# Performance work log

Measured on AMD Instinct MI355X. Metric: run time of the kernel, lower is better.

The kernel has to match this reference:

```python
import jax, jax.numpy as jnp
import numpy as np

N, D, E = 32768, 768, 8
F = 4 * D  # 3072


def setup_inputs() -> dict:
    key = jax.random.key(0)
    ks = jax.random.split(key, 8)
    scale = 0.02
    hidden_states = jax.random.normal(ks[0], (N, D), dtype=jnp.float32)
    Wg = jax.random.normal(ks[1], (E, D), dtype=jnp.float32) * scale  # gate, no bias
    W1 = jax.random.normal(ks[2], (E, F, D), dtype=jnp.float32) * scale
    b1 = jnp.zeros((E, F), dtype=jnp.float32)
    W2 = jax.random.normal(ks[3], (E, D, F), dtype=jnp.float32) * scale
    b2 = jnp.zeros((E, D), dtype=jnp.float32)
    W3 = jax.random.normal(ks[4], (E, 1, D), dtype=jnp.float32) * scale
    b3 = jnp.zeros((E, 1), dtype=jnp.float32)
    return {"hidden_states": hidden_states, "Wg": Wg, "W1": W1, "b1": b1,
            "W2": W2, "b2": b2, "W3": W3, "b3": b3, "top_k": 2}


def reference(hidden_states, Wg, W1, b1, W2, b2, W3, b3, top_k):
    x = hidden_states  # [N, D]
    logits = x @ Wg.T  # [N, E]
    probs = jax.nn.softmax(logits.astype(jnp.float32), axis=-1)
    w, _sel = jax.lax.top_k(probs, top_k)  # [N, k] (descending)
    w = (w / w.sum(axis=-1, keepdims=True)).astype(x.dtype)
    # FAITHFUL TO SOURCE BUG: expert used is the position index j (experts[j]),
    # not the selected expert id. So densely run experts 0..top_k-1 on all tokens.
    W1k, b1k = W1[:top_k], b1[:top_k]
    W2k, b2k = W2[:top_k], b2[:top_k]
    W3k, b3k = W3[:top_k], b3[:top_k]
    # dropout is identity in eval mode
    h = jax.nn.relu(jnp.einsum('nd,kfd->knf', x, W1k) + b1k[:, None, :])  # [k,N,F]
    o = x[None, :, :] + jnp.einsum('knf,kdf->knd', h, W2k) + b2k[:, None, :]  # residual, [k,N,D]
    s = jnp.einsum('knd,kod->kno', o, W3k) + b3k[:, None, :]  # [k,N,1]
    out = jnp.sum(jnp.swapaxes(w, 0, 1)[:, :, None] * s, axis=0)  # [N,1]
    return out
```

## Files before the change

kernel.cpp:

```cpp
#include <hip/hip_runtime.h>
#include <hip/hip_bf16.h>
#include <stdint.h>

#define N_TOK 32768
#define DDIM  768
#define FDIM  3072
#define NCOLS (2*FDIM)
#define BK    64
#define KTILES (DDIM/BK)
#define NTILES (NCOLS/256)
#define VD_CHUNK 96

typedef __attribute__((ext_vector_type(8))) short bf16x8;
typedef __attribute__((ext_vector_type(4))) float f32x4;

__device__ __forceinline__ unsigned short f2bf(float f) {
  unsigned u = __builtin_bit_cast(unsigned, f);
  unsigned r = (u + 0x7fffu + ((u >> 16) & 1u)) >> 16;
  return (unsigned short)r;
}

__device__ __forceinline__ void gl_lds16(const void* g, void* l) {
  __builtin_amdgcn_global_load_lds(
      (const __attribute__((address_space(1))) unsigned int*)g,
      (__attribute__((address_space(3))) unsigned int*)l, 16, 0, 0);
}

__global__ __launch_bounds__(256) void cvt_kernel(const float* __restrict__ src,
                                                  unsigned short* __restrict__ dst) {
  size_t i = ((size_t)blockIdx.x * 256 + threadIdx.x) * 4;
  float4 f = *(const float4*)(src + i);
  ushort4 u;
  u.x = f2bf(f.x); u.y = f2bf(f.y); u.z = f2bf(f.z); u.w = f2bf(f.w);
  *(ushort4*)(dst + i) = u;
}

__global__ __launch_bounds__(256) void vcalc_kernel(const float* __restrict__ W2,
                                                    const float* __restrict__ W3,
                                                    float* __restrict__ vpart) {
  __shared__ float w3s[VD_CHUNK];
  int k  = blockIdx.x / 12;
  int fb = blockIdx.x % 12;
  int db = blockIdx.y;
  if (threadIdx.x < VD_CHUNK) w3s[threadIdx.x] = W3[k*DDIM + db*VD_CHUNK + threadIdx.x];
  __syncthreads();
  int f = fb*256 + threadIdx.x;
  const float* W2k = W2 + (size_t)k*DDIM*FDIM + (size_t)db*VD_CHUNK*FDIM + f;
  float s = 0.f;
  #pragma unroll 8
  for (int d = 0; d < VD_CHUNK; ++d) s += W2k[(size_t)d*FDIM] * w3s[d];
  vpart[(size_t)db*NCOLS + k*FDIM + f] = s;
}

__global__ __launch_bounds__(256) void vfinal_kernel(const float* __restrict__ vpart,
                                                     float* __restrict__ v,
                                                     const float* __restrict__ b2,
                                                     const float* __restrict__ W3,
                                                     const float* __restrict__ b3,
                                                     float* __restrict__ cbuf) {
  int f = blockIdx.x*256 + threadIdx.x;
  float s = 0.f;
  #pragma unroll
  for (int db = 0; db < 8; ++db) s += vpart[(size_t)db*NCOLS + f];
  v[f] = s;
  if (blockIdx.x == 0 && threadIdx.x < 128) {
    int k = threadIdx.x >> 6, lane = threadIdx.x & 63;
    float c = 0.f;
    #pragma unroll
    for (int it = 0; it < DDIM/64; ++it) {
      int i = it*64 + lane;
      c += b2[k*DDIM + i] * W3[k*DDIM + i];
    }
    #pragma unroll
    for (int m = 1; m < 64; m <<= 1) c += __shfl_xor(c, m, 64);
    if (lane == 0) cbuf[k] = c + b3[k];
  }
}

__global__ __launch_bounds__(256) void gate_cvt_kernel(
    const float* __restrict__ x, const float* __restrict__ Wg,
    const float* __restrict__ W3, const float* __restrict__ cbuf,
    unsigned short* __restrict__ xbf,
    float* __restrict__ wgt, float* __restrict__ base) {
  int wid  = threadIdx.x >> 6;
  int lane = threadIdx.x & 63;
  int n = blockIdx.x * 4 + wid;
  const float4* xr = (const float4*)(x + (size_t)n * DDIM);
  ushort4* xw = (ushort4*)(xbf + (size_t)n * DDIM);
  float acc[8] = {0,0,0,0,0,0,0,0};
  float d30 = 0.f, d31 = 0.f;
  #pragma unroll
  for (int it = 0; it < DDIM/256; ++it) {
    int i = it*64 + lane;
    float4 xv = xr[i];
    ushort4 u;
    u.x = f2bf(xv.x); u.y = f2bf(xv.y); u.z = f2bf(xv.z); u.w = f2bf(xv.w);
    xw[i] = u;
    #pragma unroll
    for (int e = 0; e < 8; ++e) {
      float4 w = ((const float4*)(Wg + e*DDIM))[i];
      acc[e] += xv.x*w.x + xv.y*w.y + xv.z*w.z + xv.w*w.w;
    }
    float4 wa = ((const float4*)W3)[i];
    d30 += xv.x*wa.x + xv.y*wa.y + xv.z*wa.z + xv.w*wa.w;
    float4 wb = ((const float4*)(W3 + DDIM))[i];
    d31 += xv.x*wb.x + xv.y*wb.y + xv.z*wb.z + xv.w*wb.w;
  }
  #pragma unroll
  for (int m = 1; m < 64; m <<= 1) {
    #pragma unroll
    for (int e = 0; e < 8; ++e) acc[e] += __shfl_xor(acc[e], m, 64);
    d30 += __shfl_xor(d30, m, 64);
    d31 += __shfl_xor(d31, m, 64);
  }
  if (lane == 0) {
    float l1 = acc[0]; int a1 = 0;
    #pragma unroll
    for (int e = 1; e < 8; ++e) if (acc[e] > l1) { l1 = acc[e]; a1 = e; }
    float l2 = -3.4e38f;
    #pragma unroll
    for (int e = 0; e < 8; ++e) if (e != a1 && acc[e] > l2) l2 = acc[e];
    float w0 = 1.f / (1.f + __expf(l2 - l1));
    float w1 = 1.f - w0;
    wgt[2*n]   = w0;
    wgt[2*n+1] = w1;
    base[n] = w0 * (d30 + cbuf[0]) + w1 * (d31 + cbuf[1]);
  }
}

__global__ __launch_bounds__(512, 2) void gemm_kernel(
    const unsigned short* __restrict__ A,
    const unsigned short* __restrict__ B,
    const float* __restrict__ b1,
    const float* __restrict__ v,
    float* __restrict__ part) {
  __shared__ __align__(16) char smem[131072];

  const int tid  = threadIdx.x;
  const int lane = tid & 63, wid = tid >> 6;
  const int wm = wid >> 2, wn = wid & 3;
  const int q  = lane >> 4, cl = lane & 15;

  const int b  = blockIdx.x;
  const int L  = (b & 7) * 384 + (b >> 3);
  const int bn = L % 24;
  const int bm = L / 24;

  const unsigned short* Ab = A + (size_t)bm * 256 * DDIM;
  const unsigned short* Bb = B + (size_t)bn * 256 * DDIM;

  const size_t srow = (size_t)(wid*16 + cl) * DDIM + q*8;

  const int lb = lane * 16;
  const int aBase = wm*8192 + lb;
  const int bBase = 16384 + wn*4096 + lb;

  f32x4 zero = {0.f, 0.f, 0.f, 0.f};
  f32x4 acc[8][4];
  #pragma unroll
  for (int i = 0; i < 8; ++i)
    #pragma unroll
    for (int j = 0; j < 4; ++j) acc[i][j] = zero;

  auto stageA = [&](int t, int ks) {
    char* dst = smem + (t & 1) * 65536 + ks * 32768;
    const unsigned short* s0 = Ab + srow + t*BK + ks*32;
    gl_lds16(s0,            dst + wid*1024);
    gl_lds16(s0 + 128*DDIM, dst + 8192 + wid*1024);
  };
  auto stageB = [&](int t, int ks) {
    char* dst = smem + (t & 1) * 65536 + ks * 32768 + 16384;
    const unsigned short* s0 = Bb + srow + t*BK + ks*32;
    gl_lds16(s0,            dst + wid*1024);
    gl_lds16(s0 + 128*DDIM, dst + 8192 + wid*1024);
  };

  stageA(0, 0); stageB(0, 0);
  stageA(0, 1); stageB(0, 1);
  stageA(1, 0); stageB(1, 0);
  asm volatile("s_waitcnt vmcnt(8)" ::: "memory");
  __builtin_amdgcn_s_barrier();
  __builtin_amdgcn_sched_barrier(0);

  #pragma unroll
  for (int kt = 0; kt < KTILES; ++kt) {
    const char* ct = smem + (kt & 1) * 65536;
    bf16x8 a0[4], a1[4], bf0[4];

    #pragma unroll
    for (int n = 0; n < 4; ++n) bf0[n] = *(const bf16x8*)(ct + bBase + n*1024);
    #pragma unroll
    for (int m = 0; m < 4; ++m) a0[m] = *(const bf16x8*)(ct + aBase + m*1024);
    #pragma unroll
    for (int m = 0; m < 4; ++m) a1[m] = *(const bf16x8*)(ct + aBase + 4096 + m*1024);
    if (kt <= 10) { stageA(kt + 1, 1); stageB(kt + 1, 1); }
    __builtin_amdgcn_s_setprio(1);
    #pragma unroll
    for (int m = 0; m < 4; ++m)
      #pragma unroll
      for (int n = 0; n < 4; ++n)
        acc[m][n] = __builtin_amdgcn_mfma_f32_16x16x32_bf16(a0[m], bf0[n], acc[m][n], 0, 0, 0);
    #pragma unroll
    for (int m = 0; m < 4; ++m)
      #pragma unroll
      for (int n = 0; n < 4; ++n)
        acc[4 + m][n] = __builtin_amdgcn_mfma_f32_16x16x32_bf16(a1[m], bf0[n], acc[4 + m][n], 0, 0, 0);
    __builtin_amdgcn_s_setprio(0);
    if (kt <= 10) { asm volatile("s_waitcnt vmcnt(8)" ::: "memory"); }
    else          { asm volatile("s_waitcnt vmcnt(0)" ::: "memory"); }
    __builtin_amdgcn_s_barrier();
    __builtin_amdgcn_sched_barrier(0);

    #pragma unroll
    for (int n = 0; n < 4; ++n) bf0[n] = *(const bf16x8*)(ct + 32768 + bBase + n*1024);
    #pragma unroll
    for (int m = 0; m < 4; ++m) a0[m] = *(const bf16x8*)(ct + 32768 + aBase + m*1024);
    #pragma unroll
    for (int m = 0; m < 4; ++m) a1[m] = *(const bf16x8*)(ct + 32768 + aBase + 4096 + m*1024);
    if (kt <= 9) { stageA(kt + 2, 0); stageB(kt + 2, 0); }
    __builtin_amdgcn_s_setprio(1);
    #pragma unroll
    for (int m = 0; m < 4; ++m)
      #pragma unroll
      for (int n = 0; n < 4; ++n)
        acc[m][n] = __builtin_amdgcn_mfma_f32_16x16x32_bf16(a0[m], bf0[n], acc[m][n], 0, 0, 0);
    #pragma unroll
    for (int m = 0; m < 4; ++m)
      #pragma unroll
      for (int n = 0; n < 4; ++n)
        acc[4 + m][n] = __builtin_amdgcn_mfma_f32_16x16x32_bf16(a1[m], bf0[n], acc[4 + m][n], 0, 0, 0);
    __builtin_amdgcn_s_setprio(0);
    if (kt <= 9)       { asm volatile("s_waitcnt vmcnt(8)" ::: "memory"); }
    else if (kt == 10) { asm volatile("s_waitcnt vmcnt(4)" ::: "memory"); }
    __builtin_amdgcn_s_barrier();
    __builtin_amdgcn_sched_barrier(0);
  }

  float vv[4], bb[4];
  #pragma unroll
  for (int n = 0; n < 4; ++n) {
    int cg = bn*256 + wn*64 + n*16 + cl;
    vv[n] = v[cg];
    bb[n] = b1[cg];
  }
  float* red = (float*)smem;
  #pragma unroll
  for (int mt = 0; mt < 8; ++mt) {
    #pragma unroll
    for (int rr = 0; rr < 4; ++rr) {
      float s = 0.f;
      #pragma unroll
      for (int n = 0; n < 4; ++n) {
        float val = acc[mt][n][rr] + bb[n];
        s += fmaxf(val, 0.f) * vv[n];
      }
      #pragma unroll
      for (int msk = 1; msk < 16; msk <<= 1) s += __shfl_xor(s, msk, 64);
      if (cl == 0) red[(wm*128 + mt*16 + q*4 + rr)*4 + wn] = s;
    }
  }
  __syncthreads();
  if (tid < 256) {
    float r4 = red[tid*4] + red[tid*4+1] + red[tid*4+2] + red[tid*4+3];
    part[(size_t)bn * N_TOK + (size_t)bm*256 + tid] = r4;
  }
}

__global__ __launch_bounds__(256) void final_kernel(const float* __restrict__ part,
                                                    const float* __restrict__ wgt,
                                                    const float* __restrict__ base,
                                                    float* __restrict__ out) {
  int n = blockIdx.x * 256 + threadIdx.x;
  float s0 = 0.f, s1 = 0.f;
  #pragma unroll
  for (int t = 0; t < 12; ++t) s0 += part[(size_t)t*N_TOK + n];
  #pragma unroll
  for (int t = 12; t < 24; ++t) s1 += part[(size_t)t*N_TOK + n];
  out[n] = base[n] + wgt[2*n]*s0 + wgt[2*n+1]*s1;
}

extern "C" void kernel_launch(void* const* d_in, const int* in_sizes, int n_in,
                              void* d_out, int out_size, void* d_ws, size_t ws_size,
                              hipStream_t stream) {
  const float* x  = (const float*)d_in[0];
  const float* Wg = (const float*)d_in[1];
  const float* W1 = (const float*)d_in[2];
  const float* b1 = (const float*)d_in[3];
  const float* W2 = (const float*)d_in[4];
  const float* b2 = (const float*)d_in[5];
  const float* W3 = (const float*)d_in[6];
  const float* b3 = (const float*)d_in[7];
  float* out = (float*)d_out;

  char* ws = (char*)d_ws;
  size_t off = 0;
  auto alloc = [&](size_t bytes) -> char* {
    char* p = ws + off;
    off += (bytes + 255) & ~(size_t)255;
    return p;
  };
  unsigned short* xbf  = (unsigned short*)alloc((size_t)N_TOK * DDIM * 2);
  unsigned short* w1bf = (unsigned short*)alloc((size_t)NCOLS * DDIM * 2);
  float* vpart = (float*)alloc((size_t)8 * NCOLS * 4);
  float* v     = (float*)alloc((size_t)NCOLS * 4);
  float* cbuf  = (float*)alloc(64);
  float* wgt   = (float*)alloc((size_t)N_TOK * 2 * 4);
  float* base  = (float*)alloc((size_t)N_TOK * 4);
  float* part  = (float*)alloc((size_t)NTILES * N_TOK * 4);
  if (off > ws_size) return;

  cvt_kernel<<<(NCOLS*DDIM)/1024, 256, 0, stream>>>(W1, w1bf);
  vcalc_kernel<<<dim3(24, 8), 256, 0, stream>>>(W2, W3, vpart);
  vfinal_kernel<<<NCOLS/256, 256, 0, stream>>>(vpart, v, b2, W3, b3, cbuf);
  gate_cvt_kernel<<<N_TOK/4, 256, 0, stream>>>(x, Wg, W3, cbuf, xbf, wgt, base);
  gemm_kernel<<<3072, 512, 0, stream>>>(xbf, w1bf, b1, v, part);
  final_kernel<<<N_TOK/256, 256, 0, stream>>>(part, wgt, base, out);
}
```

Before: 626.6 us.

## Fuse prep kernels into one launch, split LDS waits in GEMM, simplify grid

```diff
diff --git a/kernel.cpp b/kernel.cpp
--- a/kernel.cpp
+++ b/kernel.cpp
@@ -11,6 +11,11 @@
 #define NTILES (NCOLS/256)
 #define VD_CHUNK 96
 
+#define CVT_BLOCKS   4608
+#define VCALC_BLOCKS 192
+#define GATE_BLOCKS  8192
+#define PREP_BLOCKS  (CVT_BLOCKS + VCALC_BLOCKS + 1 + GATE_BLOCKS)
+
 typedef __attribute__((ext_vector_type(8))) short bf16x8;
 typedef __attribute__((ext_vector_type(4))) float f32x4;
 
@@ -26,65 +31,60 @@
       (__attribute__((address_space(3))) unsigned int*)l, 16, 0, 0);
 }
 
-__global__ __launch_bounds__(256) void cvt_kernel(const float* __restrict__ src,
-                                                  unsigned short* __restrict__ dst) {
-  size_t i = ((size_t)blockIdx.x * 256 + threadIdx.x) * 4;
-  float4 f = *(const float4*)(src + i);
-  ushort4 u;
-  u.x = f2bf(f.x); u.y = f2bf(f.y); u.z = f2bf(f.z); u.w = f2bf(f.w);
-  *(ushort4*)(dst + i) = u;
-}
-
-__global__ __launch_bounds__(256) void vcalc_kernel(const float* __restrict__ W2,
-                                                    const float* __restrict__ W3,
-                                                    float* __restrict__ vpart) {
-  __shared__ float w3s[VD_CHUNK];
-  int k  = blockIdx.x / 12;
-  int fb = blockIdx.x % 12;
-  int db = blockIdx.y;
-  if (threadIdx.x < VD_CHUNK) w3s[threadIdx.x] = W3[k*DDIM + db*VD_CHUNK + threadIdx.x];
-  __syncthreads();
-  int f = fb*256 + threadIdx.x;
-  const float* W2k = W2 + (size_t)k*DDIM*FDIM + (size_t)db*VD_CHUNK*FDIM + f;
-  float s = 0.f;
-  #pragma unroll 8
-  for (int d = 0; d < VD_CHUNK; ++d) s += W2k[(size_t)d*FDIM] * w3s[d];
-  vpart[(size_t)db*NCOLS + k*FDIM + f] = s;
-}
-
-__global__ __launch_bounds__(256) void vfinal_kernel(const float* __restrict__ vpart,
-                                                     float* __restrict__ v,
-                                                     const float* __restrict__ b2,
-                                                     const float* __restrict__ W3,
-                                                     const float* __restrict__ b3,
-                                                     float* __restrict__ cbuf) {
-  int f = blockIdx.x*256 + threadIdx.x;
-  float s = 0.f;
-  #pragma unroll
-  for (int db = 0; db < 8; ++db) s += vpart[(size_t)db*NCOLS + f];
-  v[f] = s;
-  if (blockIdx.x == 0 && threadIdx.x < 128) {
-    int k = threadIdx.x >> 6, lane = threadIdx.x & 63;
-    float c = 0.f;
-    #pragma unroll
-    for (int it = 0; it < DDIM/64; ++it) {
-      int i = it*64 + lane;
-      c += b2[k*DDIM + i] * W3[k*DDIM + i];
-    }
-    #pragma unroll
-    for (int m = 1; m < 64; m <<= 1) c += __shfl_xor(c, m, 64);
-    if (lane == 0) cbuf[k] = c + b3[k];
-  }
-}
-
-__global__ __launch_bounds__(256) void gate_cvt_kernel(
+__global__ __launch_bounds__(256) void prep_kernel(
+    const float* __restrict__ W1, unsigned short* __restrict__ w1bf,
+    const float* __restrict__ W2, const float* __restrict__ W3,
+    float* __restrict__ v,
+    const float* __restrict__ b2, const float* __restrict__ b3,
+    float* __restrict__ cbuf,
     const float* __restrict__ x, const float* __restrict__ Wg,
-    const float* __restrict__ W3, const float* __restrict__ cbuf,
     unsigned short* __restrict__ xbf,
     float* __restrict__ wgt, float* __restrict__ base) {
+  __shared__ float w3s[VD_CHUNK];
+  const int b = blockIdx.x;
+
+  if (b < CVT_BLOCKS) {
+    size_t i = ((size_t)b * 256 + threadIdx.x) * 4;
+    float4 f = *(const float4*)(W1 + i);
+    ushort4 u;
+    u.x = f2bf(f.x); u.y = f2bf(f.y); u.z = f2bf(f.z); u.w = f2bf(f.w);
+    *(ushort4*)(w1bf + i) = u;
+    return;
+  }
+  if (b < CVT_BLOCKS + VCALC_BLOCKS) {
+    int vb = b - CVT_BLOCKS;
+    int k  = vb / 96;
+    int fb = (vb % 96) / 8;
+    int db = vb % 8;
+    if (threadIdx.x < VD_CHUNK) w3s[threadIdx.x] = W3[k*DDIM + db*VD_CHUNK + threadIdx.x];
+    __syncthreads();
+    int f = fb*256 + threadIdx.x;
+    const float* W2k = W2 + (size_t)k*DDIM*FDIM + (size_t)db*VD_CHUNK*FDIM + f;
+    float s = 0.f;
+    #pragma unroll 8
+    for (int d = 0; d < VD_CHUNK; ++d) s += W2k[(size_t)d*FDIM] * w3s[d];
+    atomicAdd(&v[k*FDIM + f], s);
+    return;
+  }
+  if (b == CVT_BLOCKS + VCALC_BLOCKS) {
+    if (threadIdx.x < 128) {
+      int k = threadIdx.x >> 6, lane = threadIdx.x & 63;
+      float c = 0.f;
+      #pragma unroll
+      for (int it = 0; it < DDIM/64; ++it) {
+        int i = it*64 + lane;
+        c += b2[k*DDIM + i] * W3[k*DDIM + i];
+      }
+      #pragma unroll
+      for (int m = 1; m < 64; m <<= 1) c += __shfl_xor(c, m, 64);
+      if (lane == 0) cbuf[k] = c + b3[k];
+    }
+    return;
+  }
+  int gb   = b - (CVT_BLOCKS + VCALC_BLOCKS + 1);
   int wid  = threadIdx.x >> 6;
   int lane = threadIdx.x & 63;
-  int n = blockIdx.x * 4 + wid;
+  int n = gb * 4 + wid;
   const float4* xr = (const float4*)(x + (size_t)n * DDIM);
   ushort4* xw = (ushort4*)(xbf + (size_t)n * DDIM);
   float acc[8] = {0,0,0,0,0,0,0,0};
@@ -124,7 +124,7 @@
     float w1 = 1.f - w0;
     wgt[2*n]   = w0;
     wgt[2*n+1] = w1;
-    base[n] = w0 * (d30 + cbuf[0]) + w1 * (d31 + cbuf[1]);
+    base[n] = w0 * d30 + w1 * d31;
   }
 }
 
@@ -140,11 +140,8 @@
   const int lane = tid & 63, wid = tid >> 6;
   const int wm = wid >> 2, wn = wid & 3;
   const int q  = lane >> 4, cl = lane & 15;
-
-  const int b  = blockIdx.x;
-  const int L  = (b & 7) * 384 + (b >> 3);
-  const int bn = L % 24;
-  const int bm = L / 24;
+  const int bn = blockIdx.x;
+  const int bm = blockIdx.y;
 
   const unsigned short* Ab = A + (size_t)bm * 256 * DDIM;
   const unsigned short* Bb = B + (size_t)bn * 256 * DDIM;
@@ -185,26 +182,32 @@
   #pragma unroll
   for (int kt = 0; kt < KTILES; ++kt) {
     const char* ct = smem + (kt & 1) * 65536;
-    bf16x8 a0[4], a1[4], bf0[4];
-
-    #pragma unroll
-    for (int n = 0; n < 4; ++n) bf0[n] = *(const bf16x8*)(ct + bBase + n*1024);
+    bf16x8 a0[4], a1[4], bfr[4];
+
+    #pragma unroll
+    for (int n = 0; n < 4; ++n) bfr[n] = *(const bf16x8*)(ct + bBase + n*1024);
     #pragma unroll
     for (int m = 0; m < 4; ++m) a0[m] = *(const bf16x8*)(ct + aBase + m*1024);
     #pragma unroll
     for (int m = 0; m < 4; ++m) a1[m] = *(const bf16x8*)(ct + aBase + 4096 + m*1024);
     if (kt <= 10) { stageA(kt + 1, 1); stageB(kt + 1, 1); }
+    asm volatile("s_waitcnt lgkmcnt(4)" ::: "memory");
+    __builtin_amdgcn_sched_barrier(0);
     __builtin_amdgcn_s_setprio(1);
     #pragma unroll
     for (int m = 0; m < 4; ++m)
       #pragma unroll
       for (int n = 0; n < 4; ++n)
-        acc[m][n] = __builtin_amdgcn_mfma_f32_16x16x32_bf16(a0[m], bf0[n], acc[m][n], 0, 0, 0);
+        acc[m][n] = __builtin_amdgcn_mfma_f32_16x16x32_bf16(a0[m], bfr[n], acc[m][n], 0, 0, 0);
+    __builtin_amdgcn_s_setprio(0);
+    asm volatile("s_waitcnt lgkmcnt(0)" ::: "memory");
+    __builtin_amdgcn_sched_barrier(0);
+    __builtin_amdgcn_s_setprio(1);
     #pragma unroll
     for (int m = 0; m < 4; ++m)
       #pragma unroll
       for (int n = 0; n < 4; ++n)
-        acc[4 + m][n] = __builtin_amdgcn_mfma_f32_16x16x32_bf16(a1[m], bf0[n], acc[4 + m][n], 0, 0, 0);
+        acc[4 + m][n] = __builtin_amdgcn_mfma_f32_16x16x32_bf16(a1[m], bfr[n], acc[4 + m][n], 0, 0, 0);
     __builtin_amdgcn_s_setprio(0);
     if (kt <= 10) { asm volatile("s_waitcnt vmcnt(8)" ::: "memory"); }
     else          { asm volatile("s_waitcnt vmcnt(0)" ::: "memory"); }
@@ -212,23 +215,29 @@
     __builtin_amdgcn_sched_barrier(0);
 
     #pragma unroll
-    for (int n = 0; n < 4; ++n) bf0[n] = *(const bf16x8*)(ct + 32768 + bBase + n*1024);
+    for (int n = 0; n < 4; ++n) bfr[n] = *(const bf16x8*)(ct + 32768 + bBase + n*1024);
     #pragma unroll
     for (int m = 0; m < 4; ++m) a0[m] = *(const bf16x8*)(ct + 32768 + aBase + m*1024);
     #pragma unroll
     for (int m = 0; m < 4; ++m) a1[m] = *(const bf16x8*)(ct + 32768 + aBase + 4096 + m*1024);
     if (kt <= 9) { stageA(kt + 2, 0); stageB(kt + 2, 0); }
+    asm volatile("s_waitcnt lgkmcnt(4)" ::: "memory");
+    __builtin_amdgcn_sched_barrier(0);
     __builtin_amdgcn_s_setprio(1);
     #pragma unroll
     for (int m = 0; m < 4; ++m)
       #pragma unroll
       for (int n = 0; n < 4; ++n)
-        acc[m][n] = __builtin_amdgcn_mfma_f32_16x16x32_bf16(a0[m], bf0[n], acc[m][n], 0, 0, 0);
+        acc[m][n] = __builtin_amdgcn_mfma_f32_16x16x32_bf16(a0[m], bfr[n], acc[m][n], 0, 0, 0);
+    __builtin_amdgcn_s_setprio(0);
+    asm volatile("s_waitcnt lgkmcnt(0)" ::: "memory");
+    __builtin_amdgcn_sched_barrier(0);
+    __builtin_amdgcn_s_setprio(1);
     #pragma unroll
     for (int m = 0; m < 4; ++m)
       #pragma unroll
       for (int n = 0; n < 4; ++n)
-        acc[4 + m][n] = __builtin_amdgcn_mfma_f32_16x16x32_bf16(a1[m], bf0[n], acc[4 + m][n], 0, 0, 0);
+        acc[4 + m][n] = __builtin_amdgcn_mfma_f32_16x16x32_bf16(a1[m], bfr[n], acc[4 + m][n], 0, 0, 0);
     __builtin_amdgcn_s_setprio(0);
     if (kt <= 9)       { asm volatile("s_waitcnt vmcnt(8)" ::: "memory"); }
     else if (kt == 10) { asm volatile("s_waitcnt vmcnt(4)" ::: "memory"); }
@@ -269,6 +278,7 @@
 __global__ __launch_bounds__(256) void final_kernel(const float* __restrict__ part,
                                                     const float* __restrict__ wgt,
                                                     const float* __restrict__ base,
+                                                    const float* __restrict__ cbuf,
                                                     float* __restrict__ out) {
   int n = blockIdx.x * 256 + threadIdx.x;
   float s0 = 0.f, s1 = 0.f;
@@ -276,7 +286,7 @@
   for (int t = 0; t < 12; ++t) s0 += part[(size_t)t*N_TOK + n];
   #pragma unroll
   for (int t = 12; t < 24; ++t) s1 += part[(size_t)t*N_TOK + n];
-  out[n] = base[n] + wgt[2*n]*s0 + wgt[2*n+1]*s1;
+  out[n] = base[n] + wgt[2*n]*(s0 + cbuf[0]) + wgt[2*n+1]*(s1 + cbuf[1]);
 }
 
 extern "C" void kernel_launch(void* const* d_in, const int* in_sizes, int n_in,
@@ -301,7 +311,6 @@
   };
   unsigned short* xbf  = (unsigned short*)alloc((size_t)N_TOK * DDIM * 2);
   unsigned short* w1bf = (unsigned short*)alloc((size_t)NCOLS * DDIM * 2);
-  float* vpart = (float*)alloc((size_t)8 * NCOLS * 4);
   float* v     = (float*)alloc((size_t)NCOLS * 4);
   float* cbuf  = (float*)alloc(64);
   float* wgt   = (float*)alloc((size_t)N_TOK * 2 * 4);
@@ -309,10 +318,9 @@
   float* part  = (float*)alloc((size_t)NTILES * N_TOK * 4);
   if (off > ws_size) return;
 
-  cvt_kernel<<<(NCOLS*DDIM)/1024, 256, 0, stream>>>(W1, w1bf);
-  vcalc_kernel<<<dim3(24, 8), 256, 0, stream>>>(W2, W3, vpart);
-  vfinal_kernel<<<NCOLS/256, 256, 0, stream>>>(vpart, v, b2, W3, b3, cbuf);
-  gate_cvt_kernel<<<N_TOK/4, 256, 0, stream>>>(x, Wg, W3, cbuf, xbf, wgt, base);
-  gemm_kernel<<<3072, 512, 0, stream>>>(xbf, w1bf, b1, v, part);
-  final_kernel<<<N_TOK/256, 256, 0, stream>>>(part, wgt, base, out);
-}
+  hipMemsetAsync(v, 0, (size_t)NCOLS * 4, stream);
+  prep_kernel<<<PREP_BLOCKS, 256, 0, stream>>>(W1, w1bf, W2, W3, v, b2, b3, cbuf,
+                                               x, Wg, xbf, wgt, base);
+  gemm_kernel<<<dim3(NTILES, N_TOK/256), 512, 0, stream>>>(xbf, w1bf, b1, v, part);
+  final_kernel<<<N_TOK/256, 256, 0, stream>>>(part, wgt, base, cbuf, out);
+}
```

After: 607.1 us. 3.1% less time.
